# Performance work log

Measured on AMD Instinct MI355X. Metric: run time of the kernel, lower is better.

## Reference

```python
import jax, jax.numpy as jnp
import numpy as np


def setup_inputs() -> dict:
    key = jax.random.key(0)
    ks = jax.random.split(key, 5)
    B, S, F = 32, 2048, 64
    s = lambda d: 1.0 / np.sqrt(d)
    return {
        "x": jax.random.normal(ks[0], (B, S, F), jnp.float32),
        "Wq": jax.random.normal(ks[1], (F, 24), jnp.float32) * s(F),
        "Wk": jax.random.normal(ks[2], (F, 24), jnp.float32) * s(F),
        "Wv": jax.random.normal(ks[3], (F, 32), jnp.float32) * s(F),
        "Wh": jax.random.normal(ks[4], (32, F), jnp.float32) * s(32),
    }


def reference(x, Wq, Wk, Wv, Wh):
    # x: [B, S, F]
    q = jnp.einsum("bsf,fd->bsd", x, Wq)  # [B, S, 24]
    k = jnp.einsum("bsf,fd->bsd", x, Wk)  # [B, S, 24]
    v = jnp.einsum("bsf,fd->bsd", x, Wv)  # [B, S, 32]
    a = jnp.einsum("bqd,bkd->bqk", q, k)  # [B, S, S]
    # NOTE: softmax over dim=1 (query axis), as in the original module
    a = jax.nn.softmax(a, axis=1)
    h1 = jnp.einsum("bqk,bkd->bqd", a, v)  # [B, S, 32]
    return jnp.einsum("bsd,df->bsf", h1, Wh)  # [B, S, F]
```

## Files before the change

kernel.cpp:

```cpp
#include <hip/hip_runtime.h>
#include <hip/hip_fp16.h>

#define SS 2048
#define L2E 1.44269504088896340736f

typedef _Float16 f16x4 __attribute__((ext_vector_type(4)));
typedef _Float16 f16x8 __attribute__((ext_vector_type(8)));
typedef float f32x4 __attribute__((ext_vector_type(4)));

__global__ __launch_bounds__(256) void qkv_kernel(
    const float* __restrict__ x, const float* __restrict__ Wq,
    const float* __restrict__ Wk, const float* __restrict__ Wv,
    _Float16* __restrict__ qfp, _Float16* __restrict__ kfp,
    _Float16* __restrict__ vfp)
{
    __shared__ float xsT[64 * 64];
    __shared__ float wc[64 * 96];

    int t = threadIdx.x;
    for (int i = t; i < 384; i += 256) {
        float4 v = ((const float4*)Wq)[i];
        int f = (i * 4) / 24, c = (i * 4) % 24;
        *(float4*)&wc[f * 96 + c] = v;
    }
    for (int i = t; i < 384; i += 256) {
        float4 v = ((const float4*)Wk)[i];
        int f = (i * 4) / 24, c = (i * 4) % 24;
        *(float4*)&wc[f * 96 + 24 + c] = v;
    }
    for (int i = t; i < 512; i += 256) {
        float4 v = ((const float4*)Wv)[i];
        int f = i >> 3, c = (i * 4) & 31;
        *(float4*)&wc[f * 96 + 48 + c] = v;
    }
    {
        int f = t >> 2, seg = t & 3;
        *(float4*)&wc[f * 96 + 80 + seg * 4] = (float4){0.f, 0.f, 0.f, 0.f};
    }
    long rowbase = (long)blockIdx.x * 64;
    const float4* xg = (const float4*)(x + rowbase * 64);
    for (int i = t; i < 1024; i += 256) {
        int r = i >> 4, c4 = i & 15;
        float4 v = xg[i];
        xsT[(c4 * 4 + 0) * 64 + r] = v.x;
        xsT[(c4 * 4 + 1) * 64 + r] = v.y;
        xsT[(c4 * 4 + 2) * 64 + r] = v.z;
        xsT[(c4 * 4 + 3) * 64 + r] = v.w;
    }
    __syncthreads();

    int rg = t >> 3;
    int cg = t & 7;
    float acc0[12], acc1[12];
    #pragma unroll
    for (int i = 0; i < 12; ++i) acc0[i] = acc1[i] = 0.f;

    #pragma unroll 4
    for (int f = 0; f < 64; ++f) {
        float2 xv = *(const float2*)&xsT[f * 64 + rg * 2];
        const float* wr = &wc[f * 96 + cg * 12];
        float4 wA = *(const float4*)(wr);
        float4 wB = *(const float4*)(wr + 4);
        float4 wC = *(const float4*)(wr + 8);
        float wv_[12] = {wA.x, wA.y, wA.z, wA.w, wB.x, wB.y, wB.z, wB.w,
                         wC.x, wC.y, wC.z, wC.w};
        #pragma unroll
        for (int i = 0; i < 12; ++i) {
            acc0[i] += xv.x * wv_[i];
            acc1[i] += xv.y * wv_[i];
        }
    }
    __syncthreads();
    _Float16* os = (_Float16*)wc;

    if (t < 128) {
        int reg = t >> 6, rr = t & 63;
        *(f16x8*)&os[reg * 2048 + (rr >> 4) * 512 + (48 + (rr & 15)) * 8]
            = (f16x8){0, 0, 0, 0, 0, 0, 0, 0};
    }

    #pragma unroll
    for (int j = 0; j < 2; ++j) {
        int s = rg * 2 + j, st = s >> 4;
        const float* a = j ? acc1 : acc0;
        #pragma unroll
        for (int i = 0; i < 12; ++i) {
            int c = cg * 12 + i;
            if (c < 24) {
                os[st * 512 + ((c >> 3) * 16 + (s & 15)) * 8 + (c & 7)]
                    = (_Float16)(a[i] * L2E);
            } else if (c < 48) {
                int ck = c - 24;
                os[2048 + st * 512 + ((ck >> 3) * 16 + (s & 15)) * 8 + (ck & 7)]
                    = (_Float16)a[i];
            } else if (c < 80) {
                int vd = c - 48;
                os[4096 + st * 512 + (((s >> 2) & 3) * 16 + (vd & 15)) * 8
                   + (vd >> 4) * 4 + (s & 3)] = (_Float16)a[i];
            }
        }
    }
    __syncthreads();

    long blk = blockIdx.x;
    *(f16x8*)(qfp + blk * 2048 + t * 8) = *(const f16x8*)&os[t * 8];
    *(f16x8*)(kfp + blk * 2048 + t * 8) = *(const f16x8*)&os[2048 + t * 8];
    *(f16x8*)(vfp + blk * 2048 + t * 8) = *(const f16x8*)&os[4096 + t * 8];
}

__global__ __launch_bounds__(256) void stats_kernel(
    const _Float16* __restrict__ qf, const _Float16* __restrict__ kf,
    float* __restrict__ zpart)
{
    int w = blockIdx.x;
    int b = w & 31, kb = (w >> 5) & 7, qs = w >> 8;
    int t = threadIdx.x;
    int wv = t >> 6, l = t & 63, llo = l & 15, lhi = l >> 4;

    const _Float16* kfb = kf + ((long)b * 128 + kb * 16 + wv * 4) * 512 + l * 8;
    f16x8 af[4];
    #pragma unroll
    for (int kt = 0; kt < 4; ++kt) af[kt] = *(const f16x8*)(kfb + kt * 512);

    const _Float16* qb = qf + ((long)b * 128 + qs * 16) * 512 + l * 8;
    f32x4 z[4] = {{0,0,0,0},{0,0,0,0},{0,0,0,0},{0,0,0,0}};

    #pragma unroll 4
    for (int qi = 0; qi < 16; ++qi) {
        f16x8 q0 = *(const f16x8*)(qb + qi * 512);
        #pragma unroll
        for (int kt = 0; kt < 4; ++kt) {
            f32x4 d = __builtin_amdgcn_mfma_f32_16x16x32_f16(af[kt], q0,
                        (f32x4){0.f, 0.f, 0.f, 0.f}, 0, 0, 0);
            #pragma unroll
            for (int r = 0; r < 4; ++r) z[kt][r] += __builtin_amdgcn_exp2f(d[r]);
        }
    }
    #pragma unroll
    for (int m = 1; m < 16; m <<= 1)
        #pragma unroll
        for (int kt = 0; kt < 4; ++kt)
            #pragma unroll
            for (int r = 0; r < 4; ++r) z[kt][r] += __shfl_xor(z[kt][r], m, 64);
    if (llo == 0) {
        #pragma unroll
        for (int kt = 0; kt < 4; ++kt)
            *(f32x4*)(zpart + ((long)qs * 32 + b) * SS + kb * 256 + wv * 64
                      + kt * 16 + lhi * 4) = z[kt];
    }
}

__global__ __launch_bounds__(256) void finalize_kernel(
    const float* __restrict__ zpart, float* __restrict__ wneg)
{
    int i = blockIdx.x * 256 + threadIdx.x;
    float s = 0.f;
    #pragma unroll
    for (int qs = 0; qs < 8; ++qs) s += zpart[(long)qs * 32 * SS + i];
    wneg[i] = -__builtin_amdgcn_logf(s);
}

__global__ __launch_bounds__(256, 4) void attn_out_kernel(
    const _Float16* __restrict__ qf, const _Float16* __restrict__ kf,
    const _Float16* __restrict__ vf, const float* __restrict__ wneg,
    const float* __restrict__ Wh, float* __restrict__ out)
{
    __shared__ f32x4 red[4][8][64];
    int w = blockIdx.x;
    int b = w >> 5, qblk = w & 31;
    int t = threadIdx.x;
    int wv = t >> 6, l = t & 63, llo = l & 15, lhi = l >> 4;

    const _Float16* qb = qf + ((long)b * 128 + qblk * 4) * 512 + l * 8;
    f16x8 qv[4];
    #pragma unroll
    for (int g = 0; g < 4; ++g) qv[g] = *(const f16x8*)(qb + g * 512);

    const _Float16* kg = kf + ((long)b * 128 + wv * 32) * 512 + l * 8;
    const _Float16* vg = vf + ((long)b * 128 + wv * 32) * 512 + l * 8;
    const float*    wg = wneg + (long)b * SS + wv * 512 + lhi * 4;

    f32x4 acc[4][2];
    #pragma unroll
    for (int g = 0; g < 4; ++g) {
        acc[g][0] = (f32x4){0.f, 0.f, 0.f, 0.f};
        acc[g][1] = (f32x4){0.f, 0.f, 0.f, 0.f};
    }

    #pragma unroll 2
    for (int i = 0; i < 32; ++i) {
        f16x8 kfr = *(const f16x8*)(kg + i * 512);
        float4 w4 = *(const float4*)(wg + i * 16);
        f16x8 v01 = *(const f16x8*)(vg + i * 512);
        f32x4 cw = {w4.x, w4.y, w4.z, w4.w};
        f16x4 v0 = {v01[0], v01[1], v01[2], v01[3]};
        f16x4 v1 = {v01[4], v01[5], v01[6], v01[7]};
        #pragma unroll
        for (int g = 0; g < 4; ++g) {
            f32x4 d = __builtin_amdgcn_mfma_f32_16x16x32_f16(kfr, qv[g], cw, 0, 0, 0);
            f16x4 pa;
            #pragma unroll
            for (int r = 0; r < 4; ++r) pa[r] = (_Float16)__builtin_amdgcn_exp2f(d[r]);
            acc[g][0] = __builtin_amdgcn_mfma_f32_16x16x16f16(v0, pa, acc[g][0], 0, 0, 0);
            acc[g][1] = __builtin_amdgcn_mfma_f32_16x16x16f16(v1, pa, acc[g][1], 0, 0, 0);
        }
    }

    #pragma unroll
    for (int g = 0; g < 4; ++g) {
        red[wv][g * 2][l]     = acc[g][0];
        red[wv][g * 2 + 1][l] = acc[g][1];
    }
    __syncthreads();

    f16x4 wlo, whi;
    #pragma unroll
    for (int j = 0; j < 4; ++j) {
        wlo[j] = (_Float16)Wh[(4 * lhi + j) * 64 + wv * 16 + llo];
        whi[j] = (_Float16)Wh[(16 + 4 * lhi + j) * 64 + wv * 16 + llo];
    }
    long q0 = (long)b * SS + qblk * 64;
    #pragma unroll
    for (int g = 0; g < 4; ++g) {
        f32x4 s0 = red[0][g * 2][l] + red[1][g * 2][l]
                 + red[2][g * 2][l] + red[3][g * 2][l];
        f32x4 s1 = red[0][g * 2 + 1][l] + red[1][g * 2 + 1][l]
                 + red[2][g * 2 + 1][l] + red[3][g * 2 + 1][l];
        f16x4 h0, h1;
        #pragma unroll
        for (int r = 0; r < 4; ++r) {
            h0[r] = (_Float16)s0[r];
            h1[r] = (_Float16)s1[r];
        }
        f32x4 o = __builtin_amdgcn_mfma_f32_16x16x16f16(wlo, h0,
                    (f32x4){0.f, 0.f, 0.f, 0.f}, 0, 0, 0);
        o = __builtin_amdgcn_mfma_f32_16x16x16f16(whi, h1, o, 0, 0, 0);
        *(f32x4*)(out + (q0 + g * 16 + llo) * 64 + wv * 16 + 4 * lhi) = o;
    }
}

extern "C" void kernel_launch(void* const* d_in, const int* in_sizes, int n_in,
                              void* d_out, int out_size, void* d_ws, size_t ws_size,
                              hipStream_t stream) {
    const float* x  = (const float*)d_in[0];
    const float* Wq = (const float*)d_in[1];
    const float* Wk = (const float*)d_in[2];
    const float* Wv = (const float*)d_in[3];
    const float* Wh = (const float*)d_in[4];
    float* out = (float*)d_out;

    char* ws = (char*)d_ws;
    _Float16* qf  = (_Float16*)(ws);
    _Float16* kf  = (_Float16*)(ws + (4l << 20));
    _Float16* vf  = (_Float16*)(ws + (8l << 20));
    float* wneg   = (float*)(ws + (12l << 20));
    float* zpart  = (float*)(ws + (12l << 20) + (256l << 10));

    qkv_kernel<<<1024, 256, 0, stream>>>(x, Wq, Wk, Wv, qf, kf, vf);
    stats_kernel<<<2048, 256, 0, stream>>>(qf, kf, zpart);
    finalize_kernel<<<256, 256, 0, stream>>>(zpart, wneg);
    attn_out_kernel<<<1024, 256, 0, stream>>>(qf, kf, vf, wneg, Wh, out);
}
```

Measured before the change: 81.37 us.

## Stage K/V/Q tiles through LDS with double-buffered global_load_lds in attention kernels

```diff
diff --git a/kernel.cpp b/kernel.cpp
--- a/kernel.cpp
+++ b/kernel.cpp
@@ -7,6 +7,13 @@
 typedef _Float16 f16x4 __attribute__((ext_vector_type(4)));
 typedef _Float16 f16x8 __attribute__((ext_vector_type(8)));
 typedef float f32x4 __attribute__((ext_vector_type(4)));
+
+#define GLDS16(g, l) __builtin_amdgcn_global_load_lds(                          \
+    (const __attribute__((address_space(1))) void*)(g),                         \
+    (__attribute__((address_space(3))) void*)(l), 16, 0, 0)
+#define GLDS4(g, l) __builtin_amdgcn_global_load_lds(                           \
+    (const __attribute__((address_space(1))) void*)(g),                         \
+    (__attribute__((address_space(3))) void*)(l), 4, 0, 0)
 
 __global__ __launch_bounds__(256) void qkv_kernel(
     const float* __restrict__ x, const float* __restrict__ Wq,
@@ -112,8 +119,10 @@
     const _Float16* __restrict__ qf, const _Float16* __restrict__ kf,
     float* __restrict__ zpart)
 {
+    __shared__ __align__(16) _Float16 qtile[2][2048];
     int w = blockIdx.x;
-    int b = w & 31, kb = (w >> 5) & 7, qs = w >> 8;
+    int b = w >> 6, rest = w & 63;
+    int kb = rest >> 3, qs = rest & 7;
     int t = threadIdx.x;
     int wv = t >> 6, l = t & 63, llo = l & 15, lhi = l >> 4;
 
@@ -122,18 +131,24 @@
     #pragma unroll
     for (int kt = 0; kt < 4; ++kt) af[kt] = *(const f16x8*)(kfb + kt * 512);
 
-    const _Float16* qb = qf + ((long)b * 128 + qs * 16) * 512 + l * 8;
+    const _Float16* qsrc = qf + ((long)b * 128 + qs * 16 + wv) * 512 + l * 8;
     f32x4 z[4] = {{0,0,0,0},{0,0,0,0},{0,0,0,0},{0,0,0,0}};
 
-    #pragma unroll 4
-    for (int qi = 0; qi < 16; ++qi) {
-        f16x8 q0 = *(const f16x8*)(qb + qi * 512);
-        #pragma unroll
-        for (int kt = 0; kt < 4; ++kt) {
-            f32x4 d = __builtin_amdgcn_mfma_f32_16x16x32_f16(af[kt], q0,
-                        (f32x4){0.f, 0.f, 0.f, 0.f}, 0, 0, 0);
+    GLDS16(qsrc, &qtile[0][wv * 512]);
+    for (int rnd = 0; rnd < 4; ++rnd) {
+        int cb = rnd & 1;
+        __syncthreads();
+        if (rnd < 3) GLDS16(qsrc + (rnd + 1) * 2048, &qtile[cb ^ 1][wv * 512]);
+        #pragma unroll
+        for (int fi = 0; fi < 4; ++fi) {
+            f16x8 q0 = *(const f16x8*)&qtile[cb][fi * 512 + l * 8];
             #pragma unroll
-            for (int r = 0; r < 4; ++r) z[kt][r] += __builtin_amdgcn_exp2f(d[r]);
+            for (int kt = 0; kt < 4; ++kt) {
+                f32x4 d = __builtin_amdgcn_mfma_f32_16x16x32_f16(af[kt], q0,
+                            (f32x4){0.f, 0.f, 0.f, 0.f}, 0, 0, 0);
+                #pragma unroll
+                for (int r = 0; r < 4; ++r) z[kt][r] += __builtin_amdgcn_exp2f(d[r]);
+            }
         }
     }
     #pragma unroll
@@ -160,82 +175,81 @@
     wneg[i] = -__builtin_amdgcn_logf(s);
 }
 
-__global__ __launch_bounds__(256, 4) void attn_out_kernel(
+__global__ __launch_bounds__(256) void attn_out_kernel(
     const _Float16* __restrict__ qf, const _Float16* __restrict__ kf,
     const _Float16* __restrict__ vf, const float* __restrict__ wneg,
     const float* __restrict__ Wh, float* __restrict__ out)
 {
-    __shared__ f32x4 red[4][8][64];
+    __shared__ __align__(16) _Float16 lds[2][4224];
+
     int w = blockIdx.x;
     int b = w >> 5, qblk = w & 31;
     int t = threadIdx.x;
     int wv = t >> 6, l = t & 63, llo = l & 15, lhi = l >> 4;
-
-    const _Float16* qb = qf + ((long)b * 128 + qblk * 4) * 512 + l * 8;
-    f16x8 qv[4];
-    #pragma unroll
-    for (int g = 0; g < 4; ++g) qv[g] = *(const f16x8*)(qb + g * 512);
-
-    const _Float16* kg = kf + ((long)b * 128 + wv * 32) * 512 + l * 8;
-    const _Float16* vg = vf + ((long)b * 128 + wv * 32) * 512 + l * 8;
-    const float*    wg = wneg + (long)b * SS + wv * 512 + lhi * 4;
-
-    f32x4 acc[4][2];
-    #pragma unroll
-    for (int g = 0; g < 4; ++g) {
-        acc[g][0] = (f32x4){0.f, 0.f, 0.f, 0.f};
-        acc[g][1] = (f32x4){0.f, 0.f, 0.f, 0.f};
-    }
-
-    #pragma unroll 2
-    for (int i = 0; i < 32; ++i) {
-        f16x8 kfr = *(const f16x8*)(kg + i * 512);
-        float4 w4 = *(const float4*)(wg + i * 16);
-        f16x8 v01 = *(const f16x8*)(vg + i * 512);
-        f32x4 cw = {w4.x, w4.y, w4.z, w4.w};
-        f16x4 v0 = {v01[0], v01[1], v01[2], v01[3]};
-        f16x4 v1 = {v01[4], v01[5], v01[6], v01[7]};
-        #pragma unroll
-        for (int g = 0; g < 4; ++g) {
-            f32x4 d = __builtin_amdgcn_mfma_f32_16x16x32_f16(kfr, qv[g], cw, 0, 0, 0);
+    int q0 = qblk * 64 + wv * 16;
+
+    f16x8 qfr = *(const f16x8*)(qf + ((long)b * 128 + qblk * 4 + wv) * 512 + l * 8);
+
+    f16x4 whlo[4], whhi[4];
+    #pragma unroll
+    for (int fb = 0; fb < 4; ++fb)
+        #pragma unroll
+        for (int j = 0; j < 4; ++j) {
+            whlo[fb][j] = (_Float16)Wh[(4 * lhi + j) * 64 + fb * 16 + llo];
+            whhi[fb][j] = (_Float16)Wh[(16 + 4 * lhi + j) * 64 + fb * 16 + llo];
+        }
+
+    const _Float16* kgb = kf + ((long)b * 128 + wv) * 512 + l * 8;
+    const _Float16* vgb = vf + (long)b * 65536 + wv * 512 + l * 8;
+    const float*    wgb = wneg + (long)b * SS + l;
+
+    f32x4 acc0 = {0,0,0,0}, acc1 = {0,0,0,0};
+
+    GLDS16(kgb, &lds[0][wv * 512]);
+    GLDS16(vgb, &lds[0][2048 + wv * 512]);
+    if (wv == 0) GLDS4(wgb, (float*)&lds[0][4096]);
+
+    for (int tile = 0; tile < 32; ++tile) {
+        int cb = tile & 1;
+        __syncthreads();
+        if (tile < 31) {
+            GLDS16(kgb + (long)(tile + 1) * 2048, &lds[cb ^ 1][wv * 512]);
+            GLDS16(vgb + (long)(tile + 1) * 2048, &lds[cb ^ 1][2048 + wv * 512]);
+            if (wv == 0) GLDS4(wgb + (tile + 1) * 64, (float*)&lds[cb ^ 1][4096]);
+        }
+        const _Float16* Kb = &lds[cb][0];
+        const _Float16* Vb = &lds[cb][2048];
+        const float*    Wb = (const float*)&lds[cb][4096];
+        #pragma unroll
+        for (int t4 = 0; t4 < 4; ++t4) {
+            f16x8 kfr = *(const f16x8*)(Kb + t4 * 512 + l * 8);
+            float4 w4 = *(const float4*)(Wb + t4 * 16 + lhi * 4);
+            f32x4 d = __builtin_amdgcn_mfma_f32_16x16x32_f16(kfr, qfr,
+                        (f32x4){w4.x, w4.y, w4.z, w4.w}, 0, 0, 0);
             f16x4 pa;
             #pragma unroll
             for (int r = 0; r < 4; ++r) pa[r] = (_Float16)__builtin_amdgcn_exp2f(d[r]);
-            acc[g][0] = __builtin_amdgcn_mfma_f32_16x16x16f16(v0, pa, acc[g][0], 0, 0, 0);
-            acc[g][1] = __builtin_amdgcn_mfma_f32_16x16x16f16(v1, pa, acc[g][1], 0, 0, 0);
-        }
-    }
-
-    #pragma unroll
-    for (int g = 0; g < 4; ++g) {
-        red[wv][g * 2][l]     = acc[g][0];
-        red[wv][g * 2 + 1][l] = acc[g][1];
-    }
-    __syncthreads();
-
-    f16x4 wlo, whi;
-    #pragma unroll
-    for (int j = 0; j < 4; ++j) {
-        wlo[j] = (_Float16)Wh[(4 * lhi + j) * 64 + wv * 16 + llo];
-        whi[j] = (_Float16)Wh[(16 + 4 * lhi + j) * 64 + wv * 16 + llo];
-    }
-    long q0 = (long)b * SS + qblk * 64;
-    #pragma unroll
-    for (int g = 0; g < 4; ++g) {
-        f32x4 s0 = red[0][g * 2][l] + red[1][g * 2][l]
-                 + red[2][g * 2][l] + red[3][g * 2][l];
-        f32x4 s1 = red[0][g * 2 + 1][l] + red[1][g * 2 + 1][l]
-                 + red[2][g * 2 + 1][l] + red[3][g * 2 + 1][l];
-        f16x4 h0, h1;
-        #pragma unroll
-        for (int r = 0; r < 4; ++r) {
-            h0[r] = (_Float16)s0[r];
-            h1[r] = (_Float16)s1[r];
-        }
-        f32x4 o = __builtin_amdgcn_mfma_f32_16x16x16f16(wlo, h0,
+            f16x8 v01 = *(const f16x8*)(Vb + t4 * 512 + l * 8);
+            f16x4 v0 = {v01[0], v01[1], v01[2], v01[3]};
+            f16x4 v1 = {v01[4], v01[5], v01[6], v01[7]};
+            acc0 = __builtin_amdgcn_mfma_f32_16x16x16f16(v0, pa, acc0, 0, 0, 0);
+            acc1 = __builtin_amdgcn_mfma_f32_16x16x16f16(v1, pa, acc1, 0, 0, 0);
+        }
+    }
+
+    f16x4 h0, h1;
+    #pragma unroll
+    for (int r = 0; r < 4; ++r) {
+        h0[r] = (_Float16)acc0[r];
+        h1[r] = (_Float16)acc1[r];
+    }
+    float* orow = out + ((long)b * SS + q0 + llo) * 64 + 4 * lhi;
+    #pragma unroll
+    for (int fb = 0; fb < 4; ++fb) {
+        f32x4 o = __builtin_amdgcn_mfma_f32_16x16x16f16(whlo[fb], h0,
                     (f32x4){0.f, 0.f, 0.f, 0.f}, 0, 0, 0);
-        o = __builtin_amdgcn_mfma_f32_16x16x16f16(whi, h1, o, 0, 0, 0);
-        *(f32x4*)(out + (q0 + g * 16 + llo) * 64 + wv * 16 + 4 * lhi) = o;
+        o = __builtin_amdgcn_mfma_f32_16x16x16f16(whhi[fb], h1, o, 0, 0, 0);
+        *(f32x4*)(orow + fb * 16) = o;
     }
 }
 
```

Result: slower. 86.25 us (+6.0%).
